# Kernel optimization log

Measured on AMD Instinct MI355X. Metric: run time of the kernel, lower is better.

The kernel has to match this reference:

```python
import jax, jax.numpy as jnp
import numpy as np

B, H, S, D = 2, 12, 2048, 64
TEMP = 8.0  # sqrt(d_k)


def setup_inputs() -> dict:
    key = jax.random.key(0)
    ks = jax.random.split(key, 7)
    shp = (B, H, S, D)
    mk = lambda k: jax.random.normal(k, shp, dtype=jnp.float32)
    return {
        "q_real": mk(ks[0]),
        "q_imag": mk(ks[1]),
        "k_real": mk(ks[2]),
        "k_imag": mk(ks[3]),
        "v_real": mk(ks[4]),
        "v_imag": mk(ks[5]),
        "mask": jax.random.randint(ks[6], (B, 1, S, S), 0, 2).astype(jnp.int32),
    }


def reference(q_real, q_imag, k_real, k_imag, v_real, v_imag, mask):
    # attn = | (q/T) @ conj(k)^T |  -> 4 real matmuls
    qr = q_real / TEMP
    qi = q_imag / TEMP
    # (qr + i*qi) @ (kr - i*ki)^T
    ar = (jnp.einsum('bhqd,bhkd->bhqk', qr, k_real)
          + jnp.einsum('bhqd,bhkd->bhqk', qi, k_imag))
    ai = (jnp.einsum('bhqd,bhkd->bhqk', qi, k_real)
          - jnp.einsum('bhqd,bhkd->bhqk', qr, k_imag))
    attn = jnp.sqrt(ar * ar + ai * ai)  # abs of complex scores, [B,H,S,S]
    attn = jnp.where(mask == 0, jnp.float32(-1e9), attn)
    attn = jax.nn.softmax(attn, axis=-1)  # dropout omitted (eval mode)
    out_r = jnp.einsum('bhqk,bhkd->bhqd', attn, v_real)
    out_i = jnp.einsum('bhqk,bhkd->bhqd', attn, v_imag)
    return out_r, out_i, attn
```

## Files before the change

kernel.cpp:

```cpp
#include <hip/hip_runtime.h>

#define S     2048
#define D     64
#define NH    12
#define NB    2
#define NBH   (NB*NH)
#define OUTSZ ((size_t)NBH*S*D)

#define BQ    32
#define QT    (S/BQ)
#define NBLK  (NBH*QT)

#define BQ2   16
#define QT2   (S/BQ2)
#define NBLK2 (NBH*QT2)

#define KF_OFF    0
#define KF_SZ     ((size_t)NBH*S*128*2)
#define VF_OFF    (KF_OFF + KF_SZ)
#define VF_SZ     ((size_t)2*NBH*D*S*2)
#define MQ_OFF    (VF_OFF + VF_SZ)
#define MQ_SZ     ((size_t)NB*QT*S*4)
#define WS_NEED   (MQ_OFF + MQ_SZ)

typedef __attribute__((ext_vector_type(8))) short short8;
typedef __attribute__((ext_vector_type(4))) float f32x4;

__device__ __forceinline__ unsigned short f2bf(float x){
  unsigned u = __builtin_bit_cast(unsigned, x);
  u += 0x7fffu + ((u >> 16) & 1u);
  return (unsigned short)(u >> 16);
}
__device__ __forceinline__ float bf2f(unsigned short h){
  unsigned u = ((unsigned)h) << 16;
  return __builtin_bit_cast(float, u);
}
__device__ __forceinline__ short8 pack8(const float4& a, const float4& b, float sc){
  short8 r;
  r[0]=(short)f2bf(a.x*sc); r[1]=(short)f2bf(a.y*sc);
  r[2]=(short)f2bf(a.z*sc); r[3]=(short)f2bf(a.w*sc);
  r[4]=(short)f2bf(b.x*sc); r[5]=(short)f2bf(b.y*sc);
  r[6]=(short)f2bf(b.z*sc); r[7]=(short)f2bf(b.w*sc);
  return r;
}
__device__ __forceinline__ int eoff(int row, int key){
  return ((row << 12) | (key << 1)) ^ ((row & 7) << 4);
}

__global__ __launch_bounds__(256) void conv_k(const float* __restrict__ kr,
                                              const float* __restrict__ ki,
                                              unsigned short* __restrict__ kf){
  int idx  = blockIdx.x*256 + threadIdx.x;
  int lane = idx & 63;
  int kc   = (idx >> 6) & 3;
  int eo   = (idx >> 8) & 1;
  int grp  = (idx >> 9) & 63;
  int bh   = idx >> 15;
  int key  = grp*32 + 2*(lane & 15) + eo;
  int d0   = kc*32 + (lane >> 4)*8;
  const float* src = (d0 < 64) ? kr + ((size_t)bh*S + key)*64 + d0
                               : ki + ((size_t)bh*S + key)*64 + (d0 - 64);
  float4 a = *(const float4*)(src);
  float4 b = *(const float4*)(src + 4);
  *(short8*)(kf + (size_t)idx*8) = pack8(a, b, 1.f);
}

__global__ __launch_bounds__(256) void conv_v(const float* __restrict__ vr,
                                              const float* __restrict__ vi,
                                              unsigned short* __restrict__ vf){
  __shared__ unsigned short tile[64][65];
  int bid = blockIdx.x;
  int ri  = bid / (NBH*32);
  int rem = bid % (NBH*32);
  int bh  = rem / 32;
  int s0  = (rem % 32) * 64;
  const float* vp = (ri ? vi : vr) + (size_t)bh*S*D;
  int t = threadIdx.x;
  #pragma unroll
  for (int it = 0; it < 4; it++){
    int row = (t >> 4) + it*16;
    int c4  = (t & 15) * 4;
    float4 v = *(const float4*)(vp + (size_t)(s0+row)*D + c4);
    tile[c4+0][row] = f2bf(v.x);
    tile[c4+1][row] = f2bf(v.y);
    tile[c4+2][row] = f2bf(v.z);
    tile[c4+3][row] = f2bf(v.w);
  }
  __syncthreads();
  unsigned short* dst = vf + (size_t)(ri*NBH + bh) * 4*64*64*8;
  #pragma unroll
  for (int u = 0; u < 2; u++){
    int comb = u*256 + t;
    int lane = comb & 63;
    int cp   = (comb >> 6) & 1;
    int dg   = comb >> 7;
    int c    = s0/32 + cp;
    int d    = dg*16 + (lane & 15);
    int sl   = cp*32 + (lane >> 4)*8;
    short8 o;
    #pragma unroll
    for (int j = 0; j < 8; j++) o[j] = (short)tile[d][sl + j];
    *(short8*)(dst + (((size_t)dg*64 + c)*64 + lane)*8) = o;
  }
}

__global__ __launch_bounds__(256) void conv_m(const int* __restrict__ mask,
                                              unsigned* __restrict__ mq){
  int b  = blockIdx.x >> 6;
  int qt = blockIdx.x & 63;
  int qbase = qt * BQ;
  int t = threadIdx.x;
  #pragma unroll
  for (int it = 0; it < 8; it++){
    int key = it*256 + t;
    unsigned bits = 0;
    #pragma unroll
    for (int j = 0; j < 32; j++)
      bits |= (mask[((size_t)b*S + qbase + j)*S + key] ? 1u : 0u) << j;
    mq[((size_t)b*64 + qt)*S + key] = bits;
  }
}

#define ESTRIDE 4144

__global__ __launch_bounds__(512) void cattn_merged(
    const float* __restrict__ q_real, const float* __restrict__ q_imag,
    const unsigned short* __restrict__ kf,
    const unsigned short* __restrict__ vf,
    const unsigned* __restrict__ mq,
    float* __restrict__ out)
{
  __shared__ __align__(16) char elds[BQ2*ESTRIDE];
  __shared__ float l_red[8][16];
  __shared__ float linv_lds[BQ2];

  int bid = blockIdx.x;
  int swz = (bid & 7) * (NBLK2/8) + (bid >> 3);
  int bh    = swz / QT2;
  int qt2   = swz % QT2;
  int b0    = bh / NH;
  int qbase = qt2 * BQ2;
  int rowoff = (qt2 & 1) * 16;

  int tid  = threadIdx.x;
  int w    = tid >> 6;
  int lane = tid & 63;
  int col  = lane & 15;
  int kg   = lane >> 4;

  const size_t bhSD = (size_t)bh * S * D;
  const unsigned* mqp = mq + ((size_t)b0*64 + (qt2 >> 1)) * S;

  short8 a_r[4];
  {
    const float* qrp = q_real + bhSD + (size_t)(qbase + col) * D + kg*8;
    const float* qip = q_imag + bhSD + (size_t)(qbase + col) * D + kg*8;
    a_r[0] = pack8(*(const float4*)(qrp),      *(const float4*)(qrp + 4),  0.125f);
    a_r[1] = pack8(*(const float4*)(qrp + 32), *(const float4*)(qrp + 36), 0.125f);
    a_r[2] = pack8(*(const float4*)(qip),      *(const float4*)(qip + 4),  0.125f);
    a_r[3] = pack8(*(const float4*)(qip + 32), *(const float4*)(qip + 36), 0.125f);
  }

  float lsum[4] = {0.f, 0.f, 0.f, 0.f};

  for (int t = 0; t < 8; t++){
    int grp = w*8 + t;
    const unsigned short* kb = kf + (size_t)(bh*64 + grp) * 4096;
    short8 bvA[4], bvB[4];
    #pragma unroll
    for (int kc = 0; kc < 4; kc++){
      bvA[kc] = *(const short8*)(kb + ((size_t)kc*64 + lane)*8);
      bvB[kc] = *(const short8*)(kb + ((size_t)(4+kc)*64 + lane)*8);
    }
    int keyA = grp*32 + 2*col;
    unsigned umA = mqp[keyA];
    unsigned umB = mqp[keyA + 1];

    f32x4 rA=(f32x4)(0.f), pA=(f32x4)(0.f), nA=(f32x4)(0.f);
    f32x4 rB=(f32x4)(0.f), pB=(f32x4)(0.f), nB=(f32x4)(0.f);
    #pragma unroll
    for (int kc = 0; kc < 4; kc++){
      rA = __builtin_amdgcn_mfma_f32_16x16x32_bf16(a_r[kc], bvA[kc], rA, 0, 0, 0);
      rB = __builtin_amdgcn_mfma_f32_16x16x32_bf16(a_r[kc], bvB[kc], rB, 0, 0, 0);
    }
    pA = __builtin_amdgcn_mfma_f32_16x16x32_bf16(a_r[2], bvA[0], pA, 0, 0, 0);
    pA = __builtin_amdgcn_mfma_f32_16x16x32_bf16(a_r[3], bvA[1], pA, 0, 0, 0);
    nA = __builtin_amdgcn_mfma_f32_16x16x32_bf16(a_r[0], bvA[2], nA, 0, 0, 0);
    nA = __builtin_amdgcn_mfma_f32_16x16x32_bf16(a_r[1], bvA[3], nA, 0, 0, 0);
    pB = __builtin_amdgcn_mfma_f32_16x16x32_bf16(a_r[2], bvB[0], pB, 0, 0, 0);
    pB = __builtin_amdgcn_mfma_f32_16x16x32_bf16(a_r[3], bvB[1], pB, 0, 0, 0);
    nB = __builtin_amdgcn_mfma_f32_16x16x32_bf16(a_r[0], bvB[2], nB, 0, 0, 0);
    nB = __builtin_amdgcn_mfma_f32_16x16x32_bf16(a_r[1], bvB[3], nB, 0, 0, 0);

    #pragma unroll
    for (int r = 0; r < 4; r++){
      int rowl = kg*4 + r;
      int rowb = rowoff + rowl;
      float iA = pA[r] - nA[r];
      float sA = sqrtf(rA[r]*rA[r] + iA*iA);
      float eA = ((umA >> rowb) & 1u) ? __expf(sA) : 0.f;
      float iB = pB[r] - nB[r];
      float sB = sqrtf(rB[r]*rB[r] + iB*iB);
      float eB = ((umB >> rowb) & 1u) ? __expf(sB) : 0.f;
      lsum[r] += eA + eB;
      unsigned pk = (unsigned)f2bf(eA) | ((unsigned)f2bf(eB) << 16);
      *(unsigned*)(elds + rowl*ESTRIDE + grp*64 + col*4) = pk;
    }
  }

  #pragma unroll
  for (int r = 0; r < 4; r++){
    float v = lsum[r];
    v += __shfl_xor(v, 1); v += __shfl_xor(v, 2);
    v += __shfl_xor(v, 4); v += __shfl_xor(v, 8);
    if (col == 0) l_red[w][kg*4 + r] = v;
  }
  __syncthreads();
  if (tid < BQ2){
    float s = 0.f;
    #pragma unroll
    for (int ww = 0; ww < 8; ww++) s += l_red[ww][tid];
    linv_lds[tid] = 1.f / s;
  }
  __syncthreads();

  {
    int ri = w >> 2;
    int dg = w & 3;
    const unsigned short* vbase = vf + ((size_t)(ri*NBH + bh)*4 + dg) * 64*64*8;
    f32x4 acc = (f32x4)(0.f);
    for (int win = 0; win < 64; win++){
      short8 bv = *(const short8*)(vbase + ((size_t)win*64 + lane)*8);
      short8 a  = *(const short8*)(elds + col*ESTRIDE + win*64 + kg*16);
      acc = __builtin_amdgcn_mfma_f32_16x16x32_bf16(a, bv, acc, 0, 0, 0);
    }
    float* outp = out + (ri ? OUTSZ : 0) + bhSD;
    #pragma unroll
    for (int r = 0; r < 4; r++){
      int row = kg*4 + r;
      outp[(size_t)(qbase + row) * D + dg*16 + col] = acc[r] * linv_lds[row];
    }
  }

  {
    float* attnp = out + 2*OUTSZ + (size_t)bh*S*S + (size_t)qbase*S;
    #pragma unroll 4
    for (int it = 0; it < 32; it++){
      int p   = it*512 + tid;
      int row = p >> 10;
      int po  = p & 1023;
      unsigned pk = *(const unsigned*)(elds + row*ESTRIDE + po*4);
      float inv = linv_lds[row];
      float2 o;
      o.x = bf2f((unsigned short)(pk & 0xffffu)) * inv;
      o.y = bf2f((unsigned short)(pk >> 16))     * inv;
      *(float2*)(attnp + (size_t)row*S + 2*po) = o;
    }
  }
}

__global__ __launch_bounds__(512) void cattn_kernel(
    const float* __restrict__ q_real, const float* __restrict__ q_imag,
    const float* __restrict__ k_real, const float* __restrict__ k_imag,
    const float* __restrict__ v_real, const float* __restrict__ v_imag,
    const int*   __restrict__ mask,   float* __restrict__ out)
{
  extern __shared__ __align__(16) char lds[];
  float* l_lds = (float*)(lds + (size_t)BQ*S*2);
  float* l_inv = l_lds + 8*BQ;

  int bid = blockIdx.x;
  int swz = (bid & 7) * (NBLK/8) + (bid >> 3);
  int bh    = swz / QT;
  int qt    = swz % QT;
  int b0    = bh / NH;
  int qbase = qt * BQ;

  int tid  = threadIdx.x;
  int w    = tid >> 6;
  int lane = tid & 63;
  int col  = lane & 15;
  int kg   = lane >> 4;

  const size_t bhSD = (size_t)bh * S * D;

  short8 a_r[2][4], a_i[2][4];
  #pragma unroll
  for (int m = 0; m < 2; m++){
    const float* qrp = q_real + bhSD + (size_t)(qbase + m*16 + col) * D;
    const float* qip = q_imag + bhSD + (size_t)(qbase + m*16 + col) * D;
    #pragma unroll
    for (int h = 0; h < 2; h++){
      int d0 = h*32 + kg*8;
      float4 r0 = *(const float4*)(qrp + d0);
      float4 r1 = *(const float4*)(qrp + d0 + 4);
      float4 i0 = *(const float4*)(qip + d0);
      float4 i1 = *(const float4*)(qip + d0 + 4);
      a_r[m][h]   = pack8(r0, r1,  0.125f);
      a_r[m][2+h] = pack8(i0, i1,  0.125f);
      a_i[m][h]   = a_r[m][2+h];
      a_i[m][2+h] = pack8(r0, r1, -0.125f);
    }
  }

  float lsum[2][4] = {{0.f,0.f,0.f,0.f},{0.f,0.f,0.f,0.f}};
  const int* mrow = mask + (size_t)b0 * S * S;

  for (int t = 0; t < 16; t++){
    int key = w*256 + t*16 + col;
    const float* krp = k_real + bhSD + (size_t)key * D;
    const float* kip = k_imag + bhSD + (size_t)key * D;
    short8 bv[4];
    #pragma unroll
    for (int h = 0; h < 2; h++){
      int d0 = h*32 + kg*8;
      float4 r0 = *(const float4*)(krp + d0);
      float4 r1 = *(const float4*)(krp + d0 + 4);
      float4 i0 = *(const float4*)(kip + d0);
      float4 i1 = *(const float4*)(kip + d0 + 4);
      bv[h]   = pack8(r0, r1, 1.f);
      bv[2+h] = pack8(i0, i1, 1.f);
    }
    f32x4 accr[2], acci[2];
    #pragma unroll
    for (int m = 0; m < 2; m++){ accr[m] = (f32x4)(0.f); acci[m] = (f32x4)(0.f); }
    #pragma unroll
    for (int m = 0; m < 2; m++)
      #pragma unroll
      for (int kc = 0; kc < 4; kc++){
        accr[m] = __builtin_amdgcn_mfma_f32_16x16x32_bf16(a_r[m][kc], bv[kc], accr[m], 0, 0, 0);
        acci[m] = __builtin_amdgcn_mfma_f32_16x16x32_bf16(a_i[m][kc], bv[kc], acci[m], 0, 0, 0);
      }
    #pragma unroll
    for (int m = 0; m < 2; m++){
      int qrow_g = qbase + m*16 + kg*4;
      #pragma unroll
      for (int r = 0; r < 4; r++){
        float ar = accr[m][r], ai = acci[m][r];
        float s  = sqrtf(ar*ar + ai*ai);
        int  mv  = mrow[(size_t)(qrow_g + r) * S + key];
        float ex = __expf(s);
        float e  = mv ? ex : 0.f;
        lsum[m][r] += e;
        *(unsigned short*)(lds + eoff(m*16 + kg*4 + r, key)) = f2bf(e);
      }
    }
  }

  #pragma unroll
  for (int m = 0; m < 2; m++)
    #pragma unroll
    for (int r = 0; r < 4; r++){
      float v = lsum[m][r];
      v += __shfl_xor(v, 1); v += __shfl_xor(v, 2);
      v += __shfl_xor(v, 4); v += __shfl_xor(v, 8);
      lsum[m][r] = v;
    }
  if (col == 0){
    #pragma unroll
    for (int m = 0; m < 2; m++)
      #pragma unroll
      for (int r = 0; r < 4; r++)
        l_lds[w*BQ + m*16 + kg*4 + r] = lsum[m][r];
  }
  __syncthreads();
  if (tid < BQ){
    float t = 0.f;
    #pragma unroll
    for (int ww = 0; ww < 8; ww++) t += l_lds[ww*BQ + tid];
    l_inv[tid] = 1.f / t;
  }
  __syncthreads();

  {
    int ri    = w >> 2;
    int dbase = (w & 3) * 16;
    const float* vp = (ri ? v_imag : v_real) + bhSD;
    f32x4 acc[2]; acc[0] = (f32x4)(0.f); acc[1] = (f32x4)(0.f);
    for (int c = 0; c < 64; c++){
      int k0 = c*32 + kg*8;
      short8 bv;
      #pragma unroll
      for (int j = 0; j < 8; j++)
        bv[j] = (short)f2bf(vp[(size_t)(k0 + j) * D + dbase + col]);
      #pragma unroll
      for (int m = 0; m < 2; m++){
        short8 av = *(const short8*)(lds + eoff(m*16 + col, k0));
        acc[m] = __builtin_amdgcn_mfma_f32_16x16x32_bf16(av, bv, acc[m], 0, 0, 0);
      }
    }
    float* outp = out + (ri ? OUTSZ : 0) + bhSD;
    #pragma unroll
    for (int m = 0; m < 2; m++)
      #pragma unroll
      for (int r = 0; r < 4; r++){
        int row = m*16 + kg*4 + r;
        outp[(size_t)(qbase + row) * D + dbase + col] = acc[m][r] * l_inv[row];
      }
  }

  {
    float* attnp = out + 2*OUTSZ + (size_t)bh*S*S + (size_t)qbase*S;
    #pragma unroll
    for (int g = 0; g < 16; g++){
      int flat = g*4096 + tid*8;
      int row  = flat >> 11;
      int k    = flat & 2047;
      short8 ev = *(const short8*)(lds + eoff(row, k));
      float inv = l_inv[row];
      float4 o0, o1;
      o0.x = bf2f((unsigned short)ev[0]) * inv;
      o0.y = bf2f((unsigned short)ev[1]) * inv;
      o0.z = bf2f((unsigned short)ev[2]) * inv;
      o0.w = bf2f((unsigned short)ev[3]) * inv;
      o1.x = bf2f((unsigned short)ev[4]) * inv;
      o1.y = bf2f((unsigned short)ev[5]) * inv;
      o1.z = bf2f((unsigned short)ev[6]) * inv;
      o1.w = bf2f((unsigned short)ev[7]) * inv;
      *(float4*)(attnp + (size_t)row*S + k)     = o0;
      *(float4*)(attnp + (size_t)row*S + k + 4) = o1;
    }
  }
}

extern "C" void kernel_launch(void* const* d_in, const int* in_sizes, int n_in,
                              void* d_out, int out_size, void* d_ws, size_t ws_size,
                              hipStream_t stream)
{
  const float* qr = (const float*)d_in[0];
  const float* qi = (const float*)d_in[1];
  const float* kr = (const float*)d_in[2];
  const float* ki = (const float*)d_in[3];
  const float* vr = (const float*)d_in[4];
  const float* vi = (const float*)d_in[5];
  const int*   mk = (const int*)d_in[6];
  float* out = (float*)d_out;

  if (ws_size >= WS_NEED){
    unsigned short* kf = (unsigned short*)((char*)d_ws + KF_OFF);
    unsigned short* vf = (unsigned short*)((char*)d_ws + VF_OFF);
    unsigned*       mq = (unsigned*)((char*)d_ws + MQ_OFF);
    conv_k<<<dim3(3072),     dim3(256), 0, stream>>>(kr, ki, kf);
    conv_v<<<dim3(2*NBH*32), dim3(256), 0, stream>>>(vr, vi, vf);
    conv_m<<<dim3(NB*QT),    dim3(256), 0, stream>>>(mk, mq);
    cattn_merged<<<dim3(NBLK2), dim3(512), 0, stream>>>(qr, qi, kf, vf, mq, out);
  } else {
    size_t ldsb = (size_t)BQ*S*2 + (size_t)8*BQ*4 + (size_t)BQ*4;
    cattn_kernel<<<dim3(NBLK), dim3(512), ldsb, stream>>>(qr, qi, kr, ki, vr, vi, mk, out);
  }
}
```

Before: 245.3 us.

## Merge conversion kernels and fuse attention-matrix store into PV MFMA loop

Replaces the three separate preprocessing launches (K pack, V transpose-pack, mask bitpack) with one kernel that dispatches on block index, removing two launch overheads and letting the work overlap. It also moves the write of the normalized attention probabilities into the P·V MFMA loop: the four real-part waves write each bf16 A fragment already in registers back as fp32, so the separate LDS re-read pass is dropped. The cost is divergent branches and global stores inside the MFMA loop, and fragment-shaped stores that may coalesce less well.

Result: slower. 383.2 us (+56.3%).

```diff
diff --git a/kernel.cpp b/kernel.cpp
--- a/kernel.cpp
+++ b/kernel.cpp
@@ -23,6 +23,11 @@
 #define MQ_SZ     ((size_t)NB*QT*S*4)
 #define WS_NEED   (MQ_OFF + MQ_SZ)
 
+#define CK_BLKS   3072
+#define CV_BLKS   (2*NBH*32)
+#define CM_BLKS   (NB*QT)
+#define CONV_BLKS (CK_BLKS + CV_BLKS + CM_BLKS)
+
 typedef __attribute__((ext_vector_type(8))) short short8;
 typedef __attribute__((ext_vector_type(4))) float f32x4;
 
@@ -47,77 +52,78 @@
   return ((row << 12) | (key << 1)) ^ ((row & 7) << 4);
 }
 
-__global__ __launch_bounds__(256) void conv_k(const float* __restrict__ kr,
-                                              const float* __restrict__ ki,
-                                              unsigned short* __restrict__ kf){
-  int idx  = blockIdx.x*256 + threadIdx.x;
-  int lane = idx & 63;
-  int kc   = (idx >> 6) & 3;
-  int eo   = (idx >> 8) & 1;
-  int grp  = (idx >> 9) & 63;
-  int bh   = idx >> 15;
-  int key  = grp*32 + 2*(lane & 15) + eo;
-  int d0   = kc*32 + (lane >> 4)*8;
-  const float* src = (d0 < 64) ? kr + ((size_t)bh*S + key)*64 + d0
-                               : ki + ((size_t)bh*S + key)*64 + (d0 - 64);
-  float4 a = *(const float4*)(src);
-  float4 b = *(const float4*)(src + 4);
-  *(short8*)(kf + (size_t)idx*8) = pack8(a, b, 1.f);
-}
-
-__global__ __launch_bounds__(256) void conv_v(const float* __restrict__ vr,
-                                              const float* __restrict__ vi,
-                                              unsigned short* __restrict__ vf){
-  __shared__ unsigned short tile[64][65];
-  int bid = blockIdx.x;
-  int ri  = bid / (NBH*32);
-  int rem = bid % (NBH*32);
-  int bh  = rem / 32;
-  int s0  = (rem % 32) * 64;
-  const float* vp = (ri ? vi : vr) + (size_t)bh*S*D;
-  int t = threadIdx.x;
-  #pragma unroll
-  for (int it = 0; it < 4; it++){
-    int row = (t >> 4) + it*16;
-    int c4  = (t & 15) * 4;
-    float4 v = *(const float4*)(vp + (size_t)(s0+row)*D + c4);
-    tile[c4+0][row] = f2bf(v.x);
-    tile[c4+1][row] = f2bf(v.y);
-    tile[c4+2][row] = f2bf(v.z);
-    tile[c4+3][row] = f2bf(v.w);
-  }
-  __syncthreads();
-  unsigned short* dst = vf + (size_t)(ri*NBH + bh) * 4*64*64*8;
-  #pragma unroll
-  for (int u = 0; u < 2; u++){
-    int comb = u*256 + t;
-    int lane = comb & 63;
-    int cp   = (comb >> 6) & 1;
-    int dg   = comb >> 7;
-    int c    = s0/32 + cp;
-    int d    = dg*16 + (lane & 15);
-    int sl   = cp*32 + (lane >> 4)*8;
-    short8 o;
-    #pragma unroll
-    for (int j = 0; j < 8; j++) o[j] = (short)tile[d][sl + j];
-    *(short8*)(dst + (((size_t)dg*64 + c)*64 + lane)*8) = o;
-  }
-}
-
-__global__ __launch_bounds__(256) void conv_m(const int* __restrict__ mask,
-                                              unsigned* __restrict__ mq){
-  int b  = blockIdx.x >> 6;
-  int qt = blockIdx.x & 63;
-  int qbase = qt * BQ;
-  int t = threadIdx.x;
-  #pragma unroll
-  for (int it = 0; it < 8; it++){
-    int key = it*256 + t;
-    unsigned bits = 0;
-    #pragma unroll
-    for (int j = 0; j < 32; j++)
-      bits |= (mask[((size_t)b*S + qbase + j)*S + key] ? 1u : 0u) << j;
-    mq[((size_t)b*64 + qt)*S + key] = bits;
+__global__ __launch_bounds__(256) void conv_all(
+    const float* __restrict__ kr, const float* __restrict__ ki,
+    const float* __restrict__ vr, const float* __restrict__ vi,
+    const int*   __restrict__ mask,
+    unsigned short* __restrict__ kf, unsigned short* __restrict__ vf,
+    unsigned* __restrict__ mq)
+{
+  __shared__ __align__(4) unsigned short tile[64][65];
+  int blk = blockIdx.x;
+  int t   = threadIdx.x;
+
+  if (blk < CK_BLKS){
+    int idx  = blk*256 + t;
+    int lane = idx & 63;
+    int kc   = (idx >> 6) & 3;
+    int eo   = (idx >> 8) & 1;
+    int grp  = (idx >> 9) & 63;
+    int bh   = idx >> 15;
+    int key  = grp*32 + 2*(lane & 15) + eo;
+    int d0   = kc*32 + (lane >> 4)*8;
+    const float* src = (d0 < 64) ? kr + ((size_t)bh*S + key)*64 + d0
+                                 : ki + ((size_t)bh*S + key)*64 + (d0 - 64);
+    float4 a = *(const float4*)(src);
+    float4 b = *(const float4*)(src + 4);
+    *(short8*)(kf + (size_t)idx*8) = pack8(a, b, 1.f);
+  } else if (blk < CK_BLKS + CV_BLKS){
+    int bid = blk - CK_BLKS;
+    int ri  = bid / (NBH*32);
+    int rem = bid % (NBH*32);
+    int bh  = rem / 32;
+    int s0  = (rem % 32) * 64;
+    const float* vp = (ri ? vi : vr) + (size_t)bh*S*D;
+    #pragma unroll
+    for (int it = 0; it < 4; it++){
+      int row = (t >> 4) + it*16;
+      int c4  = (t & 15) * 4;
+      float4 v = *(const float4*)(vp + (size_t)(s0+row)*D + c4);
+      tile[c4+0][row] = f2bf(v.x);
+      tile[c4+1][row] = f2bf(v.y);
+      tile[c4+2][row] = f2bf(v.z);
+      tile[c4+3][row] = f2bf(v.w);
+    }
+    __syncthreads();
+    unsigned short* dst = vf + (size_t)(ri*NBH + bh) * 4*64*64*8;
+    #pragma unroll
+    for (int u = 0; u < 2; u++){
+      int comb = u*256 + t;
+      int lane = comb & 63;
+      int cp   = (comb >> 6) & 1;
+      int dg   = comb >> 7;
+      int c    = s0/32 + cp;
+      int d    = dg*16 + (lane & 15);
+      int sl   = cp*32 + (lane >> 4)*8;
+      short8 o;
+      #pragma unroll
+      for (int j = 0; j < 8; j++) o[j] = (short)tile[d][sl + j];
+      *(short8*)(dst + (((size_t)dg*64 + c)*64 + lane)*8) = o;
+    }
+  } else {
+    int bid = blk - CK_BLKS - CV_BLKS;
+    int b   = bid >> 6;
+    int qt  = bid & 63;
+    int qbase = qt * BQ;
+    #pragma unroll
+    for (int it = 0; it < 8; it++){
+      int key = it*256 + t;
+      unsigned bits = 0;
+      #pragma unroll
+      for (int j = 0; j < 32; j++)
+        bits |= (mask[((size_t)b*S + qbase + j)*S + key] ? 1u : 0u) << j;
+      mq[((size_t)b*64 + qt)*S + key] = bits;
+    }
   }
 }
 
@@ -228,33 +234,33 @@
     int ri = w >> 2;
     int dg = w & 3;
     const unsigned short* vbase = vf + ((size_t)(ri*NBH + bh)*4 + dg) * 64*64*8;
+    float* attnp = out + 2*OUTSZ + (size_t)bh*S*S + (size_t)(qbase + col)*S + kg*8;
+    float linv_c = linv_lds[col];
     f32x4 acc = (f32x4)(0.f);
     for (int win = 0; win < 64; win++){
       short8 bv = *(const short8*)(vbase + ((size_t)win*64 + lane)*8);
       short8 a  = *(const short8*)(elds + col*ESTRIDE + win*64 + kg*16);
       acc = __builtin_amdgcn_mfma_f32_16x16x32_bf16(a, bv, acc, 0, 0, 0);
+      if (ri == 0 && (win & 3) == dg){
+        float4 o0, o1;
+        o0.x = bf2f((unsigned short)a[0]) * linv_c;
+        o0.y = bf2f((unsigned short)a[1]) * linv_c;
+        o0.z = bf2f((unsigned short)a[2]) * linv_c;
+        o0.w = bf2f((unsigned short)a[3]) * linv_c;
+        o1.x = bf2f((unsigned short)a[4]) * linv_c;
+        o1.y = bf2f((unsigned short)a[5]) * linv_c;
+        o1.z = bf2f((unsigned short)a[6]) * linv_c;
+        o1.w = bf2f((unsigned short)a[7]) * linv_c;
+        float* p = attnp + win*32;
+        *(float4*)(p)     = o0;
+        *(float4*)(p + 4) = o1;
+      }
     }
     float* outp = out + (ri ? OUTSZ : 0) + bhSD;
     #pragma unroll
     for (int r = 0; r < 4; r++){
       int row = kg*4 + r;
       outp[(size_t)(qbase + row) * D + dg*16 + col] = acc[r] * linv_lds[row];
-    }
-  }
-
-  {
-    float* attnp = out + 2*OUTSZ + (size_t)bh*S*S + (size_t)qbase*S;
-    #pragma unroll 4
-    for (int it = 0; it < 32; it++){
-      int p   = it*512 + tid;
-      int row = p >> 10;
-      int po  = p & 1023;
-      unsigned pk = *(const unsigned*)(elds + row*ESTRIDE + po*4);
-      float inv = linv_lds[row];
-      float2 o;
-      o.x = bf2f((unsigned short)(pk & 0xffffu)) * inv;
-      o.y = bf2f((unsigned short)(pk >> 16))     * inv;
-      *(float2*)(attnp + (size_t)row*S + 2*po) = o;
     }
   }
 }
@@ -440,9 +446,7 @@
     unsigned short* kf = (unsigned short*)((char*)d_ws + KF_OFF);
     unsigned short* vf = (unsigned short*)((char*)d_ws + VF_OFF);
     unsigned*       mq = (unsigned*)((char*)d_ws + MQ_OFF);
-    conv_k<<<dim3(3072),     dim3(256), 0, stream>>>(kr, ki, kf);
-    conv_v<<<dim3(2*NBH*32), dim3(256), 0, stream>>>(vr, vi, vf);
-    conv_m<<<dim3(NB*QT),    dim3(256), 0, stream>>>(mk, mq);
+    conv_all<<<dim3(CONV_BLKS), dim3(256), 0, stream>>>(kr, ki, vr, vi, mk, kf, vf, mq);
     cattn_merged<<<dim3(NBLK2), dim3(512), 0, stream>>>(qr, qi, kf, vf, mq, out);
   } else {
     size_t ldsb = (size_t)BQ*S*2 + (size_t)8*BQ*4 + (size_t)BQ*4;
```
